# Performance work log

Measured on AMD Instinct MI355X. Metric: run time of the kernel, lower is better.

## Reference

```python
import jax, jax.numpy as jnp
import numpy as np

N, E = 20000, 640000
IN_CH, IN_ECH, MID = 96, 16, 64


def _ln(x, g, b, eps=1e-5):
    mu = jnp.mean(x, axis=-1, keepdims=True)
    var = jnp.var(x, axis=-1, keepdims=True)
    return (x - mu) * jax.lax.rsqrt(var + eps) * g + b


def _conv(x, src, dst, ea, w1, b1, w2, b2, wr, t):
    # message: gather x_i (dst) / x_j (src), concat edge_attr, 2-layer MLP
    m = jnp.concatenate([x[dst], x[src], ea], axis=-1)      # [E, 3*MID]
    h = jax.nn.relu(m @ w1 + b1)                             # [E, 2*MID]
    msg = h @ w2 + b2                                        # [E, MID]
    # scatter_softmax over edges sharing a destination node (per channel)
    s = msg * t
    mx = jax.ops.segment_max(s, dst, num_segments=N)         # [N, MID]
    e = jnp.exp(s - mx[dst])
    den = jax.ops.segment_sum(e, dst, num_segments=N)
    w = e / den[dst]
    out = jax.ops.segment_sum(msg * w, dst, num_segments=N)  # [N, MID]
    out = out + x @ wr                                       # root weight (no bias)
    return out, msg


def setup_inputs() -> dict:
    key = jax.random.key(0)
    ks = jax.random.split(key, 16)

    def lin(k, fi, fo):  # xavier-normal-ish
        return jax.random.normal(k, (fi, fo), jnp.float32) * np.sqrt(2.0 / (fi + fo))

    inp = {
        "x": jax.random.normal(ks[0], (N, IN_CH), jnp.float32),
        "edge_index": jax.random.randint(ks[1], (2, E), 0, N),
        "edge_attr": jax.random.normal(ks[2], (E, IN_ECH), jnp.float32),
        # node / edge encoders: Linear + LayerNorm(affine)
        "enc_w": lin(ks[3], IN_CH, MID), "enc_b": jnp.zeros((MID,), jnp.float32),
        "enc_g": jnp.ones((MID,), jnp.float32), "enc_bb": jnp.zeros((MID,), jnp.float32),
        "eenc_w": lin(ks[4], IN_ECH, MID), "eenc_b": jnp.zeros((MID,), jnp.float32),
        "eenc_g": jnp.ones((MID,), jnp.float32), "eenc_bb": jnp.zeros((MID,), jnp.float32),
        # conv0 (bare first conv of the block)
        "c0_w1": lin(ks[5], 3 * MID, 2 * MID), "c0_b1": jnp.zeros((2 * MID,), jnp.float32),
        "c0_w2": lin(ks[6], 2 * MID, MID), "c0_b2": jnp.zeros((MID,), jnp.float32),
        "c0_wr": lin(ks[7], MID, MID), "c0_t": jnp.ones((1,), jnp.float32),
        # res+ layer: node LayerNorm + edge LayerNorm + conv1
        "l1_g": jnp.ones((MID,), jnp.float32), "l1_b": jnp.zeros((MID,), jnp.float32),
        "l1_eg": jnp.ones((MID,), jnp.float32), "l1_eb": jnp.zeros((MID,), jnp.float32),
        "c1_w1": lin(ks[8], 3 * MID, 2 * MID), "c1_b1": jnp.zeros((2 * MID,), jnp.float32),
        "c1_w2": lin(ks[9], 2 * MID, MID), "c1_b2": jnp.zeros((MID,), jnp.float32),
        "c1_wr": lin(ks[10], MID, MID), "c1_t": jnp.ones((1,), jnp.float32),
    }
    return inp


def reference(x, edge_index, edge_attr, enc_w, enc_b, enc_g, enc_bb,
              eenc_w, eenc_b, eenc_g, eenc_bb,
              c0_w1, c0_b1, c0_w2, c0_b2, c0_wr, c0_t,
              l1_g, l1_b, l1_eg, l1_eb,
              c1_w1, c1_b1, c1_w2, c1_b2, c1_wr, c1_t):
    src, dst = edge_index[0], edge_index[1]
    # encoders
    x = _ln(x @ enc_w + enc_b, enc_g, enc_bb)
    ea = _ln(edge_attr @ eenc_w + eenc_b, eenc_g, eenc_bb)
    # first conv (no norm / residual)
    x, ea = _conv(x, src, dst, ea, c0_w1, c0_b1, c0_w2, c0_b2, c0_wr, c0_t)
    # res+ layer (dropout identity in eval)
    h = jax.nn.relu(_ln(x, l1_g, l1_b))
    ean = _ln(ea, l1_eg, l1_eb)
    h, msg = _conv(h, src, dst, ean, c1_w1, c1_b1, c1_w2, c1_b2, c1_wr, c1_t)
    x = x + h  # node residual; edge stream would be ea + msg
    return x
```

## Files before the change

### kernel.cpp

```cpp
#include <hip/hip_runtime.h>

#define NN 20000
#define NE 640000
#define NTILES (NE / 64)
#define XSTR 72
#define HSTR 136

typedef float f32x4 __attribute__((ext_vector_type(4)));
typedef short short8 __attribute__((ext_vector_type(8)));
union S8I4 { int4 i; short8 s; };

#define MFMA(a, b, c) __builtin_amdgcn_mfma_f32_16x16x32_bf16((a), (b), (c), 0, 0, 0)

__device__ __forceinline__ short f2bf(float f) {
    unsigned u = __float_as_uint(f);
    u = (u + 0x7FFFu + ((u >> 16) & 1u)) >> 16;
    return (short)u;
}
__device__ __forceinline__ float bf2f(short s) {
    return __uint_as_float(((unsigned)(unsigned short)s) << 16);
}

__global__ __launch_bounds__(256) void k_prep_w(
    const float* __restrict__ w1a, const float* __restrict__ w2a,
    const float* __restrict__ w1b, const float* __restrict__ w2b,
    const float* __restrict__ eencw,
    const float* __restrict__ g0, const float* __restrict__ be0,
    const float* __restrict__ g1, const float* __restrict__ be1,
    const float* __restrict__ b1a, const float* __restrict__ b1b,
    short* __restrict__ p1a, short* __restrict__ p2a,
    short* __restrict__ p1b, short* __restrict__ p2b,
    short* __restrict__ pbenc, float* __restrict__ b1ea, float* __restrict__ b1eb)
{
    int idx = blockIdx.x * 256 + threadIdx.x;
    {
        int f = idx >> 9, l = (idx >> 3) & 63, j = idx & 7;
        int kt = f >> 3, nt = f & 7;
        int k = kt * 32 + ((l >> 4) << 3) + j;
        int n = (nt << 4) + (l & 15);
        float sa = (k >= 128) ? g0[k - 128] : 1.f;
        float sb = (k >= 128) ? g1[k - 128] : 1.f;
        p1a[idx] = f2bf(sa * w1a[k * 128 + n]);
        p1b[idx] = f2bf(sb * w1b[k * 128 + n]);
    }
    if (idx < 8192) {
        int f = idx >> 9, l = (idx >> 3) & 63, j = idx & 7;
        int kt = f >> 2, nt = f & 3;
        int k = kt * 32 + ((l >> 4) << 3) + j;
        int n = (nt << 4) + (l & 15);
        p2a[idx] = f2bf(w2a[k * 64 + n]);
        p2b[idx] = f2bf(w2b[k * 64 + n]);
    }
    if (idx < 2048) {
        int f = idx >> 9, l = (idx >> 3) & 63, j = idx & 7;
        int k = ((l >> 4) << 3) + j;
        int n = (f << 4) + (l & 15);
        pbenc[idx] = (k < 16) ? f2bf(eencw[k * 64 + n]) : (short)0;
    }
    if (idx < 256) {
        int conv = idx >> 7, j = idx & 127;
        const float* w1  = conv ? w1b : w1a;
        const float* bet = conv ? be1 : be0;
        float s = conv ? b1b[j] : b1a[j];
        for (int k = 0; k < 64; ++k) s = fmaf(bet[k], w1[(128 + k) * 128 + j], s);
        (conv ? b1eb : b1ea)[j] = s;
    }
}

__global__ __launch_bounds__(256) void k_node_enc(
    const float* __restrict__ x, const float* __restrict__ w,
    const float* __restrict__ b, const float* __restrict__ g,
    const float* __restrict__ bb, float* __restrict__ out, short* __restrict__ outb)
{
    int node = (blockIdx.x * 256 + threadIdx.x) >> 6;
    int lane = threadIdx.x & 63;
    if (node >= NN) return;
    const float* xr = x + (size_t)node * 96;
    float acc = b[lane];
    #pragma unroll
    for (int k = 0; k < 96; ++k) acc = fmaf(xr[k], w[k * 64 + lane], acc);
    float s = acc, s2 = acc * acc;
    #pragma unroll
    for (int off = 32; off; off >>= 1) { s += __shfl_xor(s, off); s2 += __shfl_xor(s2, off); }
    float mu = s * 0.015625f, var = s2 * 0.015625f - mu * mu;
    float r = rsqrtf(var + 1e-5f);
    float v = (acc - mu) * r * g[lane] + bb[lane];
    size_t idx = (size_t)node * 64 + lane;
    out[idx] = v;
    outb[idx] = f2bf(v);
}

__global__ __launch_bounds__(256) void k_degree(
    const int* __restrict__ eidx, int* __restrict__ deg)
{
    int e = blockIdx.x * 256 + threadIdx.x;
    if (e < NE) atomicAdd(&deg[eidx[NE + e]], 1);
}

__global__ __launch_bounds__(1024) void k_scan(
    const int* __restrict__ deg, int* __restrict__ row_ptr, int* __restrict__ cursor)
{
    __shared__ int sums[1024];
    const int T = 1024, CHUNK = (NN + 1023) / 1024;
    int tid = threadIdx.x;
    int base = tid * CHUNK;
    int local = 0;
    for (int i = 0; i < CHUNK; ++i) { int idx = base + i; if (idx < NN) local += deg[idx]; }
    sums[tid] = local;
    __syncthreads();
    for (int off = 1; off < T; off <<= 1) {
        int v = (tid >= off) ? sums[tid - off] : 0;
        __syncthreads();
        sums[tid] += v;
        __syncthreads();
    }
    int run = (tid == 0) ? 0 : sums[tid - 1];
    for (int i = 0; i < CHUNK; ++i) {
        int idx = base + i;
        if (idx < NN) { row_ptr[idx] = run; cursor[idx] = run; run += deg[idx]; }
    }
    if (tid == T - 1) row_ptr[NN] = run;
}

__global__ __launch_bounds__(256) void k_scatter(
    const int* __restrict__ eidx, int* __restrict__ cursor,
    int* __restrict__ psrc, int* __restrict__ pdst, int* __restrict__ peid)
{
    int e = blockIdx.x * 256 + threadIdx.x;
    if (e < NE) {
        int s = eidx[e], d = eidx[NE + e];
        int p = atomicAdd(&cursor[d], 1);
        psrc[p] = s; pdst[p] = d; peid[p] = e;
    }
}

template <int MODE>
__global__ __launch_bounds__(256, 3) void k_conv_mfma(
    const short* __restrict__ xb,
    const int* __restrict__ psrc, const int* __restrict__ pdst,
    const int* __restrict__ peid,
    const float* __restrict__ eattr,
    const short* __restrict__ pbenc,
    const float* __restrict__ encb,
    const short* __restrict__ w1p, const float* __restrict__ b1e,
    const short* __restrict__ w2p, const float* __restrict__ b2,
    short* __restrict__ msgb)
{
    __shared__ short x_lds[128 * XSTR];
    __shared__ short a_lds[64 * XSTR];
    __shared__ short h_lds[64 * HSTR];
    const int tid  = threadIdx.x;
    const int wave = tid >> 6;
    const int lane = tid & 63;
    const int quad = lane >> 4;
    const int l15  = lane & 15;
    const int qoff = quad * 8;

    short8 B1[6][2], B2[4], Benc;
    {
        const int4* p = (const int4*)w1p;
        #pragma unroll
        for (int kt = 0; kt < 6; ++kt)
            #pragma unroll
            for (int nf = 0; nf < 2; ++nf) {
                S8I4 u; u.i = p[(kt * 8 + wave * 2 + nf) * 64 + lane];
                B1[kt][nf] = u.s;
            }
        const int4* q = (const int4*)w2p;
        #pragma unroll
        for (int kt = 0; kt < 4; ++kt) { S8I4 u; u.i = q[(kt * 4 + wave) * 64 + lane]; B2[kt] = u.s; }
        if (MODE == 0) { S8I4 u; u.i = ((const int4*)pbenc)[wave * 64 + lane]; Benc = u.s; }
    }
    const float b1v0 = b1e[wave * 32 + l15];
    const float b1v1 = b1e[wave * 32 + 16 + l15];
    const float b2v  = b2[wave * 16 + l15];
    const float encbv = (MODE == 0) ? encb[wave * 16 + l15] : 0.f;

    for (int t = blockIdx.x; t < NTILES; t += gridDim.x) {
        const int ebase = t * 64;
        __syncthreads();

        #pragma unroll
        for (int it = 0; it < 4; ++it) {
            int item = it * 256 + tid;
            int row = item >> 3, c = item & 7;
            int slot = ebase + (row & 63);
            int node = (row < 64) ? pdst[slot] : psrc[slot];
            *(int4*)(x_lds + row * XSTR + c * 8) =
                *(const int4*)(xb + (size_t)node * 64 + c * 8);
        }
        if (MODE == 1) {
            #pragma unroll
            for (int it = 0; it < 2; ++it) {
                int item = it * 256 + tid;
                int row = item >> 3, c = item & 7;
                *(int4*)(a_lds + row * XSTR + c * 8) =
                    *(const int4*)(msgb + (size_t)(ebase + row) * 64 + c * 8);
            }
        } else {
            #pragma unroll
            for (int mt = 0; mt < 4; ++mt) {
                int slot = ebase + mt * 16 + l15;
                short8 ae = {0, 0, 0, 0, 0, 0, 0, 0};
                if (quad < 2) {
                    int row = peid[slot];
                    const float* ap = eattr + (size_t)row * 16 + qoff;
                    float4 u0 = *(const float4*)ap;
                    float4 u1 = *(const float4*)(ap + 4);
                    ae[0] = f2bf(u0.x); ae[1] = f2bf(u0.y); ae[2] = f2bf(u0.z); ae[3] = f2bf(u0.w);
                    ae[4] = f2bf(u1.x); ae[5] = f2bf(u1.y); ae[6] = f2bf(u1.z); ae[7] = f2bf(u1.w);
                }
                f32x4 ac = {encbv, encbv, encbv, encbv};
                ac = MFMA(ae, Benc, ac);
                #pragma unroll
                for (int r = 0; r < 4; ++r)
                    a_lds[(mt * 16 + quad * 4 + r) * XSTR + wave * 16 + l15] = f2bf(ac[r]);
            }
        }
        __syncthreads();

        {
            int m = tid >> 2, q = tid & 3;
            short* rp = a_lds + m * XSTR + q * 16;
            S8I4 u0, u1;
            u0.i = *(int4*)rp;
            u1.i = *(int4*)(rp + 8);
            float v[16], s = 0.f, s2 = 0.f;
            #pragma unroll
            for (int j = 0; j < 8; ++j) { v[j] = bf2f(u0.s[j]); v[8 + j] = bf2f(u1.s[j]); }
            #pragma unroll
            for (int j = 0; j < 16; ++j) { s += v[j]; s2 = fmaf(v[j], v[j], s2); }
            s  += __shfl_xor(s, 1);  s  += __shfl_xor(s, 2);
            s2 += __shfl_xor(s2, 1); s2 += __shfl_xor(s2, 2);
            float mu = s * 0.015625f, var = s2 * 0.015625f - mu * mu;
            float rs = rsqrtf(var + 1e-5f);
            S8I4 w0, w1u;
            #pragma unroll
            for (int j = 0; j < 8; ++j) {
                w0.s[j]  = f2bf((v[j] - mu) * rs);
                w1u.s[j] = f2bf((v[8 + j] - mu) * rs);
            }
            *(int4*)rp       = w0.i;
            *(int4*)(rp + 8) = w1u.i;
        }
        __syncthreads();

        f32x4 acc[4][2];
        #pragma unroll
        for (int mt = 0; mt < 4; ++mt) {
            acc[mt][0] = (f32x4){b1v0, b1v0, b1v0, b1v0};
            acc[mt][1] = (f32x4){b1v1, b1v1, b1v1, b1v1};
        }
        #pragma unroll
        for (int mt = 0; mt < 4; ++mt) {
            const short* xr = x_lds + (mt * 16 + l15) * XSTR;
            const short* sr = xr + 64 * XSTR;
            const short* ar = a_lds + (mt * 16 + l15) * XSTR;
            S8I4 a0, a1, a2, a3, a4, a5;
            a0.i = *(const int4*)(xr + qoff);
            a1.i = *(const int4*)(xr + 32 + qoff);
            a2.i = *(const int4*)(sr + qoff);
            a3.i = *(const int4*)(sr + 32 + qoff);
            a4.i = *(const int4*)(ar + qoff);
            a5.i = *(const int4*)(ar + 32 + qoff);
            acc[mt][0] = MFMA(a0.s, B1[0][0], acc[mt][0]);
            acc[mt][1] = MFMA(a0.s, B1[0][1], acc[mt][1]);
            acc[mt][0] = MFMA(a1.s, B1[1][0], acc[mt][0]);
            acc[mt][1] = MFMA(a1.s, B1[1][1], acc[mt][1]);
            acc[mt][0] = MFMA(a2.s, B1[2][0], acc[mt][0]);
            acc[mt][1] = MFMA(a2.s, B1[2][1], acc[mt][1]);
            acc[mt][0] = MFMA(a3.s, B1[3][0], acc[mt][0]);
            acc[mt][1] = MFMA(a3.s, B1[3][1], acc[mt][1]);
            acc[mt][0] = MFMA(a4.s, B1[4][0], acc[mt][0]);
            acc[mt][1] = MFMA(a4.s, B1[4][1], acc[mt][1]);
            acc[mt][0] = MFMA(a5.s, B1[5][0], acc[mt][0]);
            acc[mt][1] = MFMA(a5.s, B1[5][1], acc[mt][1]);
        }
        __syncthreads();

        #pragma unroll
        for (int mt = 0; mt < 4; ++mt)
            #pragma unroll
            for (int nf = 0; nf < 2; ++nf) {
                int n = wave * 32 + nf * 16 + l15;
                #pragma unroll
                for (int r = 0; r < 4; ++r) {
                    int m = mt * 16 + quad * 4 + r;
                    h_lds[m * HSTR + (n ^ (m & 8))] = f2bf(fmaxf(acc[mt][nf][r], 0.f));
                }
            }
        __syncthreads();

        f32x4 acc2[4];
        #pragma unroll
        for (int mt = 0; mt < 4; ++mt) acc2[mt] = (f32x4){b2v, b2v, b2v, b2v};
        #pragma unroll
        for (int mt = 0; mt < 4; ++mt) {
            int m = mt * 16 + l15;
            const short* hr = h_lds + m * HSTR;
            int sw = m & 8;
            #pragma unroll
            for (int kt = 0; kt < 4; ++kt) {
                S8I4 u; u.i = *(const int4*)(hr + ((kt * 32 + qoff) ^ sw));
                acc2[mt] = MFMA(u.s, B2[kt], acc2[mt]);
            }
        }
        #pragma unroll
        for (int mt = 0; mt < 4; ++mt) {
            int n = wave * 16 + l15;
            #pragma unroll
            for (int r = 0; r < 4; ++r) {
                int m = mt * 16 + quad * 4 + r;
                msgb[(size_t)(ebase + m) * 64 + n] = f2bf(acc2[mt][r]);
            }
        }
    }
}

__global__ __launch_bounds__(256) void k_gather0(
    const float* __restrict__ xenc, const short* __restrict__ msgb,
    const int* __restrict__ row_ptr,
    const float* __restrict__ wr, const float* __restrict__ g,
    const float* __restrict__ b, const float* __restrict__ tp,
    float* __restrict__ x1, short* __restrict__ hb)
{
    int node = (blockIdx.x * 256 + threadIdx.x) >> 6;
    int lane = threadIdx.x & 63;
    if (node >= NN) return;
    const float* xr = xenc + (size_t)node * 64;
    float root = 0.f;
    #pragma unroll
    for (int k = 0; k < 64; ++k) root = fmaf(xr[k], wr[k * 64 + lane], root);
    const float t = tp[0];
    int beg = row_ptr[node], end = row_ptr[node + 1];
    float den = 0.f, num = 0.f;
    for (int i = beg; i < end; ++i) {
        float m = bf2f(msgb[(size_t)i * 64 + lane]);
        float ex = __expf(m * t);
        den += ex;
        num = fmaf(m, ex, num);
    }
    float v = root + (den > 0.f ? num / den : 0.f);
    size_t idx = (size_t)node * 64 + lane;
    x1[idx] = v;
    float s = v, s2 = v * v;
    #pragma unroll
    for (int off = 32; off; off >>= 1) { s += __shfl_xor(s, off); s2 += __shfl_xor(s2, off); }
    float mu = s * 0.015625f, var = s2 * 0.015625f - mu * mu;
    float r = rsqrtf(var + 1e-5f);
    hb[idx] = f2bf(fmaxf((v - mu) * r * g[lane] + b[lane], 0.f));
}

__global__ __launch_bounds__(256) void k_gather1(
    const float* __restrict__ x1, const short* __restrict__ hb,
    const short* __restrict__ msgb, const int* __restrict__ row_ptr,
    const float* __restrict__ wr, const float* __restrict__ tp,
    float* __restrict__ out)
{
    int node = (blockIdx.x * 256 + threadIdx.x) >> 6;
    int lane = threadIdx.x & 63;
    if (node >= NN) return;
    const short* hr = hb + (size_t)node * 64;
    float root = 0.f;
    #pragma unroll
    for (int k = 0; k < 64; ++k) root = fmaf(bf2f(hr[k]), wr[k * 64 + lane], root);
    const float t = tp[0];
    int beg = row_ptr[node], end = row_ptr[node + 1];
    float den = 0.f, num = 0.f;
    for (int i = beg; i < end; ++i) {
        float m = bf2f(msgb[(size_t)i * 64 + lane]);
        float ex = __expf(m * t);
        den += ex;
        num = fmaf(m, ex, num);
    }
    size_t idx = (size_t)node * 64 + lane;
    out[idx] = x1[idx] + root + (den > 0.f ? num / den : 0.f);
}

extern "C" void kernel_launch(void* const* d_in, const int* in_sizes, int n_in,
                              void* d_out, int out_size, void* d_ws, size_t ws_size,
                              hipStream_t stream)
{
    const float* x       = (const float*)d_in[0];
    const int*   eidx    = (const int*)  d_in[1];
    const float* eattr   = (const float*)d_in[2];
    const float* enc_w   = (const float*)d_in[3];
    const float* enc_b   = (const float*)d_in[4];
    const float* enc_g   = (const float*)d_in[5];
    const float* enc_bb  = (const float*)d_in[6];
    const float* eenc_w  = (const float*)d_in[7];
    const float* eenc_b  = (const float*)d_in[8];
    const float* eenc_g  = (const float*)d_in[9];
    const float* eenc_bb = (const float*)d_in[10];
    const float* c0_w1   = (const float*)d_in[11];
    const float* c0_b1   = (const float*)d_in[12];
    const float* c0_w2   = (const float*)d_in[13];
    const float* c0_b2   = (const float*)d_in[14];
    const float* c0_wr   = (const float*)d_in[15];
    const float* c0_t    = (const float*)d_in[16];
    const float* l1_g    = (const float*)d_in[17];
    const float* l1_b    = (const float*)d_in[18];
    const float* l1_eg   = (const float*)d_in[19];
    const float* l1_eb   = (const float*)d_in[20];
    const float* c1_w1   = (const float*)d_in[21];
    const float* c1_b1   = (const float*)d_in[22];
    const float* c1_w2   = (const float*)d_in[23];
    const float* c1_b2   = (const float*)d_in[24];
    const float* c1_wr   = (const float*)d_in[25];
    const float* c1_t    = (const float*)d_in[26];

    const size_t NV = (size_t)NN * 64;
    char* base = (char*)d_ws;
    auto take = [&](size_t bytes) {
        char* p = base;
        base += (bytes + 255) & ~(size_t)255;
        return p;
    };
    float* xenc    = (float*)take(NV * 4);
    float* x1      = (float*)take(NV * 4);
    int*   deg     = (int*)  take(NN * 4);
    int*   row_ptr = (int*)  take((NN + 1) * 4);
    int*   cursor  = (int*)  take(NN * 4);
    int*   psrc    = (int*)  take((size_t)NE * 4);
    int*   pdst    = (int*)  take((size_t)NE * 4);
    int*   peid    = (int*)  take((size_t)NE * 4);
    short* xb      = (short*)take(NV * 2);
    short* hb      = (short*)take(NV * 2);
    short* w1p0    = (short*)take(24576 * 2);
    short* w1p1    = (short*)take(24576 * 2);
    short* w2p0    = (short*)take(8192 * 2);
    short* w2p1    = (short*)take(8192 * 2);
    short* pbenc   = (short*)take(2048 * 2);
    float* b1e0    = (float*)take(128 * 4);
    float* b1e1    = (float*)take(128 * 4);
    short* msgb    = (short*)take((size_t)NE * 64 * 2);
    float* out     = (float*)d_out;

    hipMemsetAsync(deg, 0, NN * sizeof(int), stream);

    k_prep_w  <<<96, 256, 0, stream>>>(c0_w1, c0_w2, c1_w1, c1_w2, eenc_w,
                                       eenc_g, eenc_bb, l1_eg, l1_eb, c0_b1, c1_b1,
                                       w1p0, w2p0, w1p1, w2p1, pbenc, b1e0, b1e1);
    k_node_enc<<<NN / 4, 256, 0, stream>>>(x, enc_w, enc_b, enc_g, enc_bb, xenc, xb);
    k_degree  <<<NE / 256, 256, 0, stream>>>(eidx, deg);
    k_scan    <<<1, 1024, 0, stream>>>(deg, row_ptr, cursor);
    k_scatter <<<NE / 256, 256, 0, stream>>>(eidx, cursor, psrc, pdst, peid);

    k_conv_mfma<0><<<768, 256, 0, stream>>>(
        xb, psrc, pdst, peid, eattr, pbenc, eenc_b,
        w1p0, b1e0, w2p0, c0_b2, msgb);

    k_gather0<<<NN / 4, 256, 0, stream>>>(
        xenc, msgb, row_ptr, c0_wr, l1_g, l1_b, c0_t, x1, hb);

    k_conv_mfma<1><<<768, 256, 0, stream>>>(
        hb, psrc, pdst, nullptr, nullptr, nullptr, nullptr,
        w1p1, b1e1, w2p1, c1_b2, msgb);

    k_gather1<<<NN / 4, 256, 0, stream>>>(
        x1, hb, msgb, row_ptr, c1_wr, c1_t, out);
}
```

Measured before the change: 633.4 us.

## Fuse setup kernels, alias conv LDS for higher occupancy, vectorize gather aggregation

Three setup kernels (weight prep, node encoder, degree count) become one launch, which cuts launch overhead. The conv kernel now overlaps the h buffer with the x buffer in LDS and stores per-row LayerNorm statistics instead of normalizing in place. That saves a barrier and LDS space, so occupancy can rise to 4 blocks per SM with a 1024-block grid. The gather kernels now have each wave process four edges at once using 8-byte loads and shuffle reductions. The costs are extra register pressure from recomputing normalization inside the MFMA loop and more complex gather code.

Measured after the change: 916.6 us. 1.45x slower.

```diff
diff --git a/kernel.cpp b/kernel.cpp
--- a/kernel.cpp
+++ b/kernel.cpp
@@ -21,80 +21,80 @@
     return __uint_as_float(((unsigned)(unsigned short)s) << 16);
 }
 
-__global__ __launch_bounds__(256) void k_prep_w(
+__global__ __launch_bounds__(256) void k_pre(
+    const float* __restrict__ x, const int* __restrict__ eidx,
+    const float* __restrict__ enc_w, const float* __restrict__ enc_b,
+    const float* __restrict__ enc_g, const float* __restrict__ enc_bb,
     const float* __restrict__ w1a, const float* __restrict__ w2a,
     const float* __restrict__ w1b, const float* __restrict__ w2b,
     const float* __restrict__ eencw,
     const float* __restrict__ g0, const float* __restrict__ be0,
     const float* __restrict__ g1, const float* __restrict__ be1,
     const float* __restrict__ b1a, const float* __restrict__ b1b,
+    float* __restrict__ xenc, short* __restrict__ xb, int* __restrict__ deg,
     short* __restrict__ p1a, short* __restrict__ p2a,
     short* __restrict__ p1b, short* __restrict__ p2b,
     short* __restrict__ pbenc, float* __restrict__ b1ea, float* __restrict__ b1eb)
 {
-    int idx = blockIdx.x * 256 + threadIdx.x;
+    const int bid = blockIdx.x, tid = threadIdx.x;
     {
-        int f = idx >> 9, l = (idx >> 3) & 63, j = idx & 7;
-        int kt = f >> 3, nt = f & 7;
-        int k = kt * 32 + ((l >> 4) << 3) + j;
-        int n = (nt << 4) + (l & 15);
-        float sa = (k >= 128) ? g0[k - 128] : 1.f;
-        float sb = (k >= 128) ? g1[k - 128] : 1.f;
-        p1a[idx] = f2bf(sa * w1a[k * 128 + n]);
-        p1b[idx] = f2bf(sb * w1b[k * 128 + n]);
-    }
-    if (idx < 8192) {
-        int f = idx >> 9, l = (idx >> 3) & 63, j = idx & 7;
-        int kt = f >> 2, nt = f & 3;
-        int k = kt * 32 + ((l >> 4) << 3) + j;
-        int n = (nt << 4) + (l & 15);
-        p2a[idx] = f2bf(w2a[k * 64 + n]);
-        p2b[idx] = f2bf(w2b[k * 64 + n]);
-    }
-    if (idx < 2048) {
-        int f = idx >> 9, l = (idx >> 3) & 63, j = idx & 7;
-        int k = ((l >> 4) << 3) + j;
-        int n = (f << 4) + (l & 15);
-        pbenc[idx] = (k < 16) ? f2bf(eencw[k * 64 + n]) : (short)0;
-    }
-    if (idx < 256) {
-        int conv = idx >> 7, j = idx & 127;
-        const float* w1  = conv ? w1b : w1a;
-        const float* bet = conv ? be1 : be0;
-        float s = conv ? b1b[j] : b1a[j];
-        for (int k = 0; k < 64; ++k) s = fmaf(bet[k], w1[(128 + k) * 128 + j], s);
-        (conv ? b1eb : b1ea)[j] = s;
-    }
-}
-
-__global__ __launch_bounds__(256) void k_node_enc(
-    const float* __restrict__ x, const float* __restrict__ w,
-    const float* __restrict__ b, const float* __restrict__ g,
-    const float* __restrict__ bb, float* __restrict__ out, short* __restrict__ outb)
-{
-    int node = (blockIdx.x * 256 + threadIdx.x) >> 6;
-    int lane = threadIdx.x & 63;
-    if (node >= NN) return;
-    const float* xr = x + (size_t)node * 96;
-    float acc = b[lane];
-    #pragma unroll
-    for (int k = 0; k < 96; ++k) acc = fmaf(xr[k], w[k * 64 + lane], acc);
-    float s = acc, s2 = acc * acc;
-    #pragma unroll
-    for (int off = 32; off; off >>= 1) { s += __shfl_xor(s, off); s2 += __shfl_xor(s2, off); }
-    float mu = s * 0.015625f, var = s2 * 0.015625f - mu * mu;
-    float r = rsqrtf(var + 1e-5f);
-    float v = (acc - mu) * r * g[lane] + bb[lane];
-    size_t idx = (size_t)node * 64 + lane;
-    out[idx] = v;
-    outb[idx] = f2bf(v);
-}
-
-__global__ __launch_bounds__(256) void k_degree(
-    const int* __restrict__ eidx, int* __restrict__ deg)
-{
-    int e = blockIdx.x * 256 + threadIdx.x;
-    if (e < NE) atomicAdd(&deg[eidx[NE + e]], 1);
+        int node = bid * 4 + (tid >> 6);
+        int lane = tid & 63;
+        if (node < NN) {
+            const float* xr = x + (size_t)node * 96;
+            float acc = enc_b[lane];
+            #pragma unroll
+            for (int k = 0; k < 96; ++k) acc = fmaf(xr[k], enc_w[k * 64 + lane], acc);
+            float s = acc, s2 = acc * acc;
+            #pragma unroll
+            for (int off = 32; off; off >>= 1) { s += __shfl_xor(s, off); s2 += __shfl_xor(s2, off); }
+            float mu = s * 0.015625f, var = s2 * 0.015625f - mu * mu;
+            float r = rsqrtf(var + 1e-5f);
+            float v = (acc - mu) * r * enc_g[lane] + enc_bb[lane];
+            size_t idx = (size_t)node * 64 + lane;
+            xenc[idx] = v;
+            xb[idx] = f2bf(v);
+        }
+    }
+    if (bid < 2500) {
+        int e = bid * 256 + tid;
+        atomicAdd(&deg[eidx[NE + e]], 1);
+    }
+    if (bid < 96) {
+        int idx = bid * 256 + tid;
+        {
+            int f = idx >> 9, l = (idx >> 3) & 63, j = idx & 7;
+            int kt = f >> 3, nt = f & 7;
+            int k = kt * 32 + ((l >> 4) << 3) + j;
+            int n = (nt << 4) + (l & 15);
+            float sa = (k >= 128) ? g0[k - 128] : 1.f;
+            float sb = (k >= 128) ? g1[k - 128] : 1.f;
+            p1a[idx] = f2bf(sa * w1a[k * 128 + n]);
+            p1b[idx] = f2bf(sb * w1b[k * 128 + n]);
+        }
+        if (idx < 8192) {
+            int f = idx >> 9, l = (idx >> 3) & 63, j = idx & 7;
+            int kt = f >> 2, nt = f & 3;
+            int k = kt * 32 + ((l >> 4) << 3) + j;
+            int n = (nt << 4) + (l & 15);
+            p2a[idx] = f2bf(w2a[k * 64 + n]);
+            p2b[idx] = f2bf(w2b[k * 64 + n]);
+        }
+        if (idx < 2048) {
+            int f = idx >> 9, l = (idx >> 3) & 63, j = idx & 7;
+            int k = ((l >> 4) << 3) + j;
+            int n = (f << 4) + (l & 15);
+            pbenc[idx] = (k < 16) ? f2bf(eencw[k * 64 + n]) : (short)0;
+        }
+        if (idx < 256) {
+            int conv = idx >> 7, j = idx & 127;
+            const float* w1  = conv ? w1b : w1a;
+            const float* bet = conv ? be1 : be0;
+            float s = conv ? b1b[j] : b1a[j];
+            for (int k = 0; k < 64; ++k) s = fmaf(bet[k], w1[(128 + k) * 128 + j], s);
+            (conv ? b1eb : b1ea)[j] = s;
+        }
+    }
 }
 
 __global__ __launch_bounds__(1024) void k_scan(
@@ -135,7 +135,7 @@
 }
 
 template <int MODE>
-__global__ __launch_bounds__(256, 3) void k_conv_mfma(
+__global__ __launch_bounds__(256, 4) void k_conv_mfma(
     const short* __restrict__ xb,
     const int* __restrict__ psrc, const int* __restrict__ pdst,
     const int* __restrict__ peid,
@@ -146,9 +146,11 @@
     const short* __restrict__ w2p, const float* __restrict__ b2,
     short* __restrict__ msgb)
 {
-    __shared__ short x_lds[128 * XSTR];
-    __shared__ short a_lds[64 * XSTR];
-    __shared__ short h_lds[64 * HSTR];
+    __shared__ short smem[192 * XSTR];
+    __shared__ float2 stats[64];
+    short* x_lds = smem;
+    short* a_lds = smem + 128 * XSTR;
+    short* h_lds = smem;
     const int tid  = threadIdx.x;
     const int wave = tid >> 6;
     const int lane = tid & 63;
@@ -194,8 +196,18 @@
             for (int it = 0; it < 2; ++it) {
                 int item = it * 256 + tid;
                 int row = item >> 3, c = item & 7;
-                *(int4*)(a_lds + row * XSTR + c * 8) =
-                    *(const int4*)(msgb + (size_t)(ebase + row) * 64 + c * 8);
+                S8I4 u;
+                u.i = *(const int4*)(msgb + (size_t)(ebase + row) * 64 + c * 8);
+                *(int4*)(a_lds + row * XSTR + c * 8) = u.i;
+                float s = 0.f, s2 = 0.f;
+                #pragma unroll
+                for (int j = 0; j < 8; ++j) {
+                    float v = bf2f(u.s[j]);
+                    s += v; s2 = fmaf(v, v, s2);
+                }
+                s  += __shfl_xor(s, 1);  s  += __shfl_xor(s, 2);  s  += __shfl_xor(s, 4);
+                s2 += __shfl_xor(s2, 1); s2 += __shfl_xor(s2, 2); s2 += __shfl_xor(s2, 4);
+                if ((tid & 7) == 0) stats[row] = make_float2(s, s2);
             }
         } else {
             #pragma unroll
@@ -219,31 +231,24 @@
         }
         __syncthreads();
 
-        {
+        if (MODE == 0) {
             int m = tid >> 2, q = tid & 3;
-            short* rp = a_lds + m * XSTR + q * 16;
+            const short* rp = a_lds + m * XSTR + q * 16;
             S8I4 u0, u1;
-            u0.i = *(int4*)rp;
-            u1.i = *(int4*)(rp + 8);
-            float v[16], s = 0.f, s2 = 0.f;
-            #pragma unroll
-            for (int j = 0; j < 8; ++j) { v[j] = bf2f(u0.s[j]); v[8 + j] = bf2f(u1.s[j]); }
-            #pragma unroll
-            for (int j = 0; j < 16; ++j) { s += v[j]; s2 = fmaf(v[j], v[j], s2); }
+            u0.i = *(const int4*)rp;
+            u1.i = *(const int4*)(rp + 8);
+            float s = 0.f, s2 = 0.f;
+            #pragma unroll
+            for (int j = 0; j < 8; ++j) {
+                float v0 = bf2f(u0.s[j]), v1 = bf2f(u1.s[j]);
+                s += v0 + v1;
+                s2 = fmaf(v0, v0, fmaf(v1, v1, s2));
+            }
             s  += __shfl_xor(s, 1);  s  += __shfl_xor(s, 2);
             s2 += __shfl_xor(s2, 1); s2 += __shfl_xor(s2, 2);
-            float mu = s * 0.015625f, var = s2 * 0.015625f - mu * mu;
-            float rs = rsqrtf(var + 1e-5f);
-            S8I4 w0, w1u;
-            #pragma unroll
-            for (int j = 0; j < 8; ++j) {
-                w0.s[j]  = f2bf((v[j] - mu) * rs);
-                w1u.s[j] = f2bf((v[8 + j] - mu) * rs);
-            }
-            *(int4*)rp       = w0.i;
-            *(int4*)(rp + 8) = w1u.i;
-        }
-        __syncthreads();
+            if (q == 0) stats[m] = make_float2(s, s2);
+            __syncthreads();
+        }
 
         f32x4 acc[4][2];
         #pragma unroll
@@ -256,13 +261,23 @@
             const short* xr = x_lds + (mt * 16 + l15) * XSTR;
             const short* sr = xr + 64 * XSTR;
             const short* ar = a_lds + (mt * 16 + l15) * XSTR;
-            S8I4 a0, a1, a2, a3, a4, a5;
+            float2 sv = stats[mt * 16 + l15];
+            float mu = sv.x * 0.015625f, var = sv.y * 0.015625f - mu * mu;
+            float rs = rsqrtf(var + 1e-5f);
+            float nb = -mu * rs;
+            S8I4 a0, a1, a2, a3, r4, r5;
             a0.i = *(const int4*)(xr + qoff);
             a1.i = *(const int4*)(xr + 32 + qoff);
             a2.i = *(const int4*)(sr + qoff);
             a3.i = *(const int4*)(sr + 32 + qoff);
-            a4.i = *(const int4*)(ar + qoff);
-            a5.i = *(const int4*)(ar + 32 + qoff);
+            r4.i = *(const int4*)(ar + qoff);
+            r5.i = *(const int4*)(ar + 32 + qoff);
+            short8 a4, a5;
+            #pragma unroll
+            for (int j = 0; j < 8; ++j) {
+                a4[j] = f2bf(fmaf(bf2f(r4.s[j]), rs, nb));
+                a5[j] = f2bf(fmaf(bf2f(r5.s[j]), rs, nb));
+            }
             acc[mt][0] = MFMA(a0.s, B1[0][0], acc[mt][0]);
             acc[mt][1] = MFMA(a0.s, B1[0][1], acc[mt][1]);
             acc[mt][0] = MFMA(a1.s, B1[1][0], acc[mt][0]);
@@ -271,10 +286,10 @@
             acc[mt][1] = MFMA(a2.s, B1[2][1], acc[mt][1]);
             acc[mt][0] = MFMA(a3.s, B1[3][0], acc[mt][0]);
             acc[mt][1] = MFMA(a3.s, B1[3][1], acc[mt][1]);
-            acc[mt][0] = MFMA(a4.s, B1[4][0], acc[mt][0]);
-            acc[mt][1] = MFMA(a4.s, B1[4][1], acc[mt][1]);
-            acc[mt][0] = MFMA(a5.s, B1[5][0], acc[mt][0]);
-            acc[mt][1] = MFMA(a5.s, B1[5][1], acc[mt][1]);
+            acc[mt][0] = MFMA(a4, B1[4][0], acc[mt][0]);
+            acc[mt][1] = MFMA(a4, B1[4][1], acc[mt][1]);
+            acc[mt][0] = MFMA(a5, B1[5][0], acc[mt][0]);
+            acc[mt][1] = MFMA(a5, B1[5][1], acc[mt][1]);
         }
         __syncthreads();
 
@@ -317,6 +332,44 @@
     }
 }
 
+__device__ __forceinline__ float gather_agg(
+    const short* __restrict__ msgb, int beg, int end, float t, int lane)
+{
+    const int cl = lane & 15, gq = lane >> 4;
+    float den0 = 0.f, den1 = 0.f, den2 = 0.f, den3 = 0.f;
+    float num0 = 0.f, num1 = 0.f, num2 = 0.f, num3 = 0.f;
+    for (int i = beg + gq; i < end; i += 4) {
+        int2 u = *(const int2*)(msgb + (size_t)i * 64 + cl * 4);
+        float m0 = bf2f((short)(u.x & 0xffff));
+        float m1 = bf2f((short)(u.x >> 16));
+        float m2 = bf2f((short)(u.y & 0xffff));
+        float m3 = bf2f((short)(u.y >> 16));
+        float e0 = __expf(m0 * t), e1 = __expf(m1 * t);
+        float e2 = __expf(m2 * t), e3 = __expf(m3 * t);
+        den0 += e0; num0 = fmaf(m0, e0, num0);
+        den1 += e1; num1 = fmaf(m1, e1, num1);
+        den2 += e2; num2 = fmaf(m2, e2, num2);
+        den3 += e3; num3 = fmaf(m3, e3, num3);
+    }
+    den0 += __shfl_xor(den0, 16); den0 += __shfl_xor(den0, 32);
+    den1 += __shfl_xor(den1, 16); den1 += __shfl_xor(den1, 32);
+    den2 += __shfl_xor(den2, 16); den2 += __shfl_xor(den2, 32);
+    den3 += __shfl_xor(den3, 16); den3 += __shfl_xor(den3, 32);
+    num0 += __shfl_xor(num0, 16); num0 += __shfl_xor(num0, 32);
+    num1 += __shfl_xor(num1, 16); num1 += __shfl_xor(num1, 32);
+    num2 += __shfl_xor(num2, 16); num2 += __shfl_xor(num2, 32);
+    num3 += __shfl_xor(num3, 16); num3 += __shfl_xor(num3, 32);
+    const int srcl = lane >> 2;
+    float dA = __shfl(den0, srcl), dB = __shfl(den1, srcl);
+    float dC = __shfl(den2, srcl), dD = __shfl(den3, srcl);
+    float nA = __shfl(num0, srcl), nB = __shfl(num1, srcl);
+    float nC = __shfl(num2, srcl), nD = __shfl(num3, srcl);
+    const int e = lane & 3;
+    float den = (e & 2) ? ((e & 1) ? dD : dC) : ((e & 1) ? dB : dA);
+    float num = (e & 2) ? ((e & 1) ? nD : nC) : ((e & 1) ? nB : nA);
+    return den > 0.f ? num / den : 0.f;
+}
+
 __global__ __launch_bounds__(256) void k_gather0(
     const float* __restrict__ xenc, const short* __restrict__ msgb,
     const int* __restrict__ row_ptr,
@@ -324,23 +377,15 @@
     const float* __restrict__ b, const float* __restrict__ tp,
     float* __restrict__ x1, short* __restrict__ hb)
 {
-    int node = (blockIdx.x * 256 + threadIdx.x) >> 6;
-    int lane = threadIdx.x & 63;
+    const int wave = threadIdx.x >> 6, lane = threadIdx.x & 63;
+    const int node = blockIdx.x * 4 + wave;
     if (node >= NN) return;
     const float* xr = xenc + (size_t)node * 64;
     float root = 0.f;
     #pragma unroll
     for (int k = 0; k < 64; ++k) root = fmaf(xr[k], wr[k * 64 + lane], root);
-    const float t = tp[0];
-    int beg = row_ptr[node], end = row_ptr[node + 1];
-    float den = 0.f, num = 0.f;
-    for (int i = beg; i < end; ++i) {
-        float m = bf2f(msgb[(size_t)i * 64 + lane]);
-        float ex = __expf(m * t);
-        den += ex;
-        num = fmaf(m, ex, num);
-    }
-    float v = root + (den > 0.f ? num / den : 0.f);
+    float agg = gather_agg(msgb, row_ptr[node], row_ptr[node + 1], tp[0], lane);
+    float v = root + agg;
     size_t idx = (size_t)node * 64 + lane;
     x1[idx] = v;
     float s = v, s2 = v * v;
@@ -357,24 +402,16 @@
     const float* __restrict__ wr, const float* __restrict__ tp,
     float* __restrict__ out)
 {
-    int node = (blockIdx.x * 256 + threadIdx.x) >> 6;
-    int lane = threadIdx.x & 63;
+    const int wave = threadIdx.x >> 6, lane = threadIdx.x & 63;
+    const int node = blockIdx.x * 4 + wave;
     if (node >= NN) return;
     const short* hr = hb + (size_t)node * 64;
     float root = 0.f;
     #pragma unroll
     for (int k = 0; k < 64; ++k) root = fmaf(bf2f(hr[k]), wr[k * 64 + lane], root);
-    const float t = tp[0];
-    int beg = row_ptr[node], end = row_ptr[node + 1];
-    float den = 0.f, num = 0.f;
-    for (int i = beg; i < end; ++i) {
-        float m = bf2f(msgb[(size_t)i * 64 + lane]);
-        float ex = __expf(m * t);
-        den += ex;
-        num = fmaf(m, ex, num);
-    }
+    float agg = gather_agg(msgb, row_ptr[node], row_ptr[node + 1], tp[0], lane);
     size_t idx = (size_t)node * 64 + lane;
-    out[idx] = x1[idx] + root + (den > 0.f ? num / den : 0.f);
+    out[idx] = x1[idx] + root + agg;
 }
 
 extern "C" void kernel_launch(void* const* d_in, const int* in_sizes, int n_in,
@@ -438,22 +475,22 @@
 
     hipMemsetAsync(deg, 0, NN * sizeof(int), stream);
 
-    k_prep_w  <<<96, 256, 0, stream>>>(c0_w1, c0_w2, c1_w1, c1_w2, eenc_w,
-                                       eenc_g, eenc_bb, l1_eg, l1_eb, c0_b1, c1_b1,
-                                       w1p0, w2p0, w1p1, w2p1, pbenc, b1e0, b1e1);
-    k_node_enc<<<NN / 4, 256, 0, stream>>>(x, enc_w, enc_b, enc_g, enc_bb, xenc, xb);
-    k_degree  <<<NE / 256, 256, 0, stream>>>(eidx, deg);
-    k_scan    <<<1, 1024, 0, stream>>>(deg, row_ptr, cursor);
-    k_scatter <<<NE / 256, 256, 0, stream>>>(eidx, cursor, psrc, pdst, peid);
-
-    k_conv_mfma<0><<<768, 256, 0, stream>>>(
+    k_pre<<<NN / 4, 256, 0, stream>>>(
+        x, eidx, enc_w, enc_b, enc_g, enc_bb,
+        c0_w1, c0_w2, c1_w1, c1_w2, eenc_w,
+        eenc_g, eenc_bb, l1_eg, l1_eb, c0_b1, c1_b1,
+        xenc, xb, deg, w1p0, w2p0, w1p1, w2p1, pbenc, b1e0, b1e1);
+    k_scan   <<<1, 1024, 0, stream>>>(deg, row_ptr, cursor);
+    k_scatter<<<NE / 256, 256, 0, stream>>>(eidx, cursor, psrc, pdst, peid);
+
+    k_conv_mfma<0><<<1024, 256, 0, stream>>>(
         xb, psrc, pdst, peid, eattr, pbenc, eenc_b,
         w1p0, b1e0, w2p0, c0_b2, msgb);
 
     k_gather0<<<NN / 4, 256, 0, stream>>>(
         xenc, msgb, row_ptr, c0_wr, l1_g, l1_b, c0_t, x1, hb);
 
-    k_conv_mfma<1><<<768, 256, 0, stream>>>(
+    k_conv_mfma<1><<<1024, 256, 0, stream>>>(
         hb, psrc, pdst, nullptr, nullptr, nullptr, nullptr,
         w1p1, b1e1, w2p1, c1_b2, msgb);
 
```
